# Kernel optimization log

Measured on AMD Instinct MI355X. Metric: run time of the kernel, lower is better.

The kernel has to match this reference:

```python
import jax, jax.numpy as jnp
import numpy as np

B, T, D = 16, 1024, 512      # batch, query time, model hidden
C = 4096                     # context entries
DC = 512                     # context hidden
A = 512                      # attndim
P = 512                      # proj hidden


def setup_inputs() -> dict:
    key = jax.random.key(0)
    ks = jax.random.split(key, 10)
    s = lambda fan_in: 1.0 / np.sqrt(fan_in)
    return {
        "model_embed": jax.random.normal(ks[0], (B, T, D), jnp.float32),
        "context_embed": jax.random.normal(ks[1], (C, DC), jnp.float32),
        "Wq": jax.random.uniform(ks[2], (D, A), jnp.float32, -s(D), s(D)),
        "bq": jax.random.uniform(ks[3], (A,), jnp.float32, -s(D), s(D)),
        "Wk": jax.random.uniform(ks[4], (DC, A), jnp.float32, -s(DC), s(DC)),
        "bk": jax.random.uniform(ks[5], (A,), jnp.float32, -s(DC), s(DC)),
        "Wv": jax.random.uniform(ks[6], (DC, A), jnp.float32, -s(DC), s(DC)),
        "bv": jax.random.uniform(ks[7], (A,), jnp.float32, -s(DC), s(DC)),
        "Wo": jax.random.uniform(ks[8], (A, P), jnp.float32, -s(A), s(A)),
        "bo": jax.random.uniform(ks[9], (P,), jnp.float32, -s(A), s(A)),
    }


def reference(model_embed, context_embed, Wq, bq, Wk, bk, Wv, bv, Wo, bo):
    q = model_embed @ Wq + bq            # [B, T, A]
    k = context_embed @ Wk + bk          # [C, A]
    v = context_embed @ Wv + bv          # [C, A]
    scale = 1.0 / jnp.sqrt(jnp.asarray(q.shape[-1], q.dtype))
    scores = jnp.einsum('ck,btk->btc', k, q) * scale   # [B, T, C]
    attn = jax.nn.softmax(scores, axis=-1)             # softmax over context
    x = jnp.einsum('ck,btc->btk', v, attn)             # [B, T, A]
    return x @ Wo + bo                                 # [B, T, P]
```

## Files before the change

### kernel.cpp

```cpp
#include <hip/hip_runtime.h>

#define MB_T 16384
#define DD   512
#define CC   4096
#define AA   512
#define PP   512

typedef __attribute__((ext_vector_type(4))) float f32x4;
typedef __attribute__((ext_vector_type(8))) short short8;

#define MFMA16(a, b, c) __builtin_amdgcn_mfma_f32_16x16x32_bf16((a), (b), (c), 0, 0, 0)

__device__ __forceinline__ unsigned short f2bf(float f) {
  union { float f; unsigned int u; } cv; cv.f = f;
  unsigned int u = cv.u;
  return (unsigned short)((u + 0x7FFFu + ((u >> 16) & 1u)) >> 16);
}
__device__ __forceinline__ float bf2f(unsigned short u) {
  union { unsigned int i; float f; } c; c.i = (unsigned int)u << 16; return c.f;
}

__device__ __forceinline__ void gload16(const unsigned short* g, unsigned short* l) {
  __builtin_amdgcn_global_load_lds(
      (const __attribute__((address_space(1))) unsigned int*)g,
      (__attribute__((address_space(3))) unsigned int*)l, 16, 0, 0);
}

__global__ void cast_bf16_kernel(const float* __restrict__ in,
                                 unsigned short* __restrict__ out, int n4) {
  int i = blockIdx.x * blockDim.x + threadIdx.x;
  int stride = gridDim.x * blockDim.x;
  for (; i < n4; i += stride) {
    float4 v = reinterpret_cast<const float4*>(in)[i];
    ushort4 o;
    o.x = f2bf(v.x); o.y = f2bf(v.y); o.z = f2bf(v.z); o.w = f2bf(v.w);
    reinterpret_cast<ushort4*>(out)[i] = o;
  }
}

__global__ __launch_bounds__(256) void transpose_cast_kernel(
    const float* __restrict__ W, unsigned short* __restrict__ WT, int rows, int cols) {
  __shared__ float t_s[32][33];
  int bi = blockIdx.y * 32, bj = blockIdx.x * 32;
  int r = threadIdx.x >> 3, c4 = (threadIdx.x & 7) * 4;
  float4 v = *reinterpret_cast<const float4*>(W + (size_t)(bi + r) * cols + bj + c4);
  t_s[r][c4 + 0] = v.x; t_s[r][c4 + 1] = v.y;
  t_s[r][c4 + 2] = v.z; t_s[r][c4 + 3] = v.w;
  __syncthreads();
  ushort4 o;
  o.x = f2bf(t_s[c4 + 0][r]);
  o.y = f2bf(t_s[c4 + 1][r]);
  o.z = f2bf(t_s[c4 + 2][r]);
  o.w = f2bf(t_s[c4 + 3][r]);
  *reinterpret_cast<ushort4*>(WT + (size_t)(bj + r) * rows + bi + c4) = o;
}

__global__ __launch_bounds__(256) void rowdot_kernel(
    const unsigned short* __restrict__ mat, const float* __restrict__ vec,
    float* __restrict__ outv, float scale) {
  const int lane = threadIdx.x & 63, wid = threadIdx.x >> 6;
  const int row = blockIdx.x * 4 + wid;
  const unsigned short* kr = mat + (size_t)row * 512 + lane * 8;
  float s = 0.f;
  ushort4 a = *reinterpret_cast<const ushort4*>(kr);
  ushort4 b = *reinterpret_cast<const ushort4*>(kr + 4);
  const float* bqp = vec + lane * 8;
  s += bf2f(a.x) * bqp[0]; s += bf2f(a.y) * bqp[1];
  s += bf2f(a.z) * bqp[2]; s += bf2f(a.w) * bqp[3];
  s += bf2f(b.x) * bqp[4]; s += bf2f(b.y) * bqp[5];
  s += bf2f(b.z) * bqp[6]; s += bf2f(b.w) * bqp[7];
#pragma unroll
  for (int d = 1; d < 64; d <<= 1) s += __shfl_xor(s, d);
  if (lane == 0) outv[row] = s * scale;
}

__global__ __launch_bounds__(256) void reduce_lsum_kernel(
    const float* __restrict__ lsp, float* __restrict__ lsum) {
  int m = blockIdx.x * blockDim.x + threadIdx.x;
  const float4* p = reinterpret_cast<const float4*>(lsp + (size_t)m * 64);
  float s = 0.f;
#pragma unroll
  for (int j = 0; j < 16; ++j) { float4 v = p[j]; s += v.x + v.y + v.z + v.w; }
  lsum[m] = s;
}

template <int MODE, int TM>
__global__ __launch_bounds__(256, 4) void gemm2p_kernel(
    const unsigned short* __restrict__ A, const unsigned short* __restrict__ BT,
    const float* __restrict__ bias, const float* __restrict__ colbias,
    const float* __restrict__ rowsum_in, float* __restrict__ psum_out,
    void* __restrict__ Cout, int M, int N, int K, float alpha) {
  constexpr int MFR = TM / 32;
  constexpr int WROW = TM / 2;
  constexpr int ASZ = TM * 32;
  constexpr int BSZ = 128 * 32;
  constexpr int STG = 2 * ASZ + 2 * BSZ;
  constexpr int TOT = (MODE == 3 && STG < 128 * 136) ? 128 * 136 : STG;
  __shared__ unsigned short lds[TOT];

  const int tid = threadIdx.x;
  const int lane = tid & 63, wid = tid >> 6;
  const int hq = lane >> 4, lq = lane & 15;
  const int wm = wid >> 1, wn = wid & 1;

  const int gx = gridDim.x;
  const int nwg = gx * gridDim.y;
  const int orig = blockIdx.y * gx + blockIdx.x;
  const int swz = (orig & 7) * (nwg >> 3) + (orig >> 3);
  const int bx = swz % gx, by = swz / gx;
  const int brow = by * TM, bcol = bx * 128;

  const unsigned short* ap = A + (size_t)(brow + (tid >> 2)) * K + (tid & 3) * 8;
  const unsigned short* bp = BT + (size_t)(bcol + (tid >> 2)) * K + (tid & 3) * 8;
  const size_t row64 = (size_t)64 * K;

  const int nt = K >> 5;
#pragma unroll
  for (int j = 0; j < TM / 64; ++j)
    gload16(ap + j * row64, lds + wid * 512 + j * 2048);
  gload16(bp, lds + 2 * ASZ + wid * 512);
  gload16(bp + row64, lds + 2 * ASZ + wid * 512 + 2048);
  __syncthreads();

  f32x4 acc[MFR][4] = {};
  for (int t = 0; t < nt; ++t) {
    const int cur = t & 1;
    if (t + 1 < nt) {
      const int k0 = (t + 1) * 32;
      unsigned short* an = lds + (cur ^ 1) * ASZ + wid * 512;
      unsigned short* bn = lds + 2 * ASZ + (cur ^ 1) * BSZ + wid * 512;
#pragma unroll
      for (int j = 0; j < TM / 64; ++j)
        gload16(ap + k0 + j * row64, an + j * 2048);
      gload16(bp + k0, bn);
      gload16(bp + k0 + row64, bn + 2048);
    }
    const unsigned short* as0 = lds + cur * ASZ;
    const unsigned short* bs0 = lds + 2 * ASZ + cur * BSZ;
    short8 af[MFR], bfv[4];
#pragma unroll
    for (int mf = 0; mf < MFR; ++mf)
      af[mf] = *reinterpret_cast<const short8*>(&as0[(wm * WROW + mf * 16 + lq) * 32 + hq * 8]);
#pragma unroll
    for (int nf = 0; nf < 4; ++nf)
      bfv[nf] = *reinterpret_cast<const short8*>(&bs0[(wn * 64 + nf * 16 + lq) * 32 + hq * 8]);
#pragma unroll
    for (int mf = 0; mf < MFR; ++mf)
#pragma unroll
      for (int nf = 0; nf < 4; ++nf)
        acc[mf][nf] = MFMA16(af[mf], bfv[nf], acc[mf][nf]);
    if (t + 1 < nt) __syncthreads();
  }

  if (MODE == 3) {
    float cb[4];
#pragma unroll
    for (int nf = 0; nf < 4; ++nf) cb[nf] = colbias[bcol + wn * 64 + nf * 16 + lq];
    __syncthreads();
#pragma unroll
    for (int mf = 0; mf < MFR; ++mf)
#pragma unroll
      for (int i = 0; i < 4; ++i) {
        const int rowl = wm * WROW + mf * 16 + hq * 4 + i;
        float s = 0.f;
#pragma unroll
        for (int nf = 0; nf < 4; ++nf) {
          float p = __expf(acc[mf][nf][i] + cb[nf]);
          s += p;
          lds[rowl * 136 + wn * 64 + nf * 16 + lq] = f2bf(p);
        }
        s += __shfl_xor(s, 1);
        s += __shfl_xor(s, 2);
        s += __shfl_xor(s, 4);
        s += __shfl_xor(s, 8);
        if (lq == 0) psum_out[(size_t)(brow + rowl) * 64 + bx * 2 + wn] = s;
      }
    __syncthreads();
#pragma unroll
    for (int j = 0; j < 8; ++j) {
      const int chunk = j * 256 + tid;
      const int row = chunk >> 4, c = chunk & 15;
      short8 v = *reinterpret_cast<const short8*>(&lds[row * 136 + c * 8]);
      *reinterpret_cast<short8*>((unsigned short*)Cout + (size_t)(brow + row) * N + bcol + c * 8) = v;
    }
  } else if (MODE == 5) {
#pragma unroll
    for (int mf = 0; mf < MFR; ++mf)
#pragma unroll
      for (int i = 0; i < 4; ++i) {
        const int rowg = brow + wm * WROW + mf * 16 + hq * 4 + i;
        const float inv = 1.0f / rowsum_in[rowg];
#pragma unroll
        for (int nf = 0; nf < 4; ++nf) {
          const int colg = bcol + wn * 64 + nf * 16 + lq;
          ((float*)Cout)[(size_t)rowg * N + colg] = acc[mf][nf][i] * inv + bias[colg];
        }
      }
  } else if (MODE == 1) {
#pragma unroll
    for (int nf = 0; nf < 4; ++nf) {
      const int colg = bcol + wn * 64 + nf * 16 + lq;
      const float bv = bias ? bias[colg] : 0.f;
#pragma unroll
      for (int mf = 0; mf < MFR; ++mf) {
        const int rowg0 = brow + wm * WROW + mf * 16 + hq * 4;
        ushort4 pk;
        pk.x = f2bf(acc[mf][nf][0] + bv);
        pk.y = f2bf(acc[mf][nf][1] + bv);
        pk.z = f2bf(acc[mf][nf][2] + bv);
        pk.w = f2bf(acc[mf][nf][3] + bv);
        *reinterpret_cast<ushort4*>((unsigned short*)Cout + (size_t)colg * M + rowg0) = pk;
      }
    }
  } else {
#pragma unroll
    for (int nf = 0; nf < 4; ++nf) {
      const int colg = bcol + wn * 64 + nf * 16 + lq;
      const float bv = bias ? bias[colg] : 0.f;
#pragma unroll
      for (int mf = 0; mf < MFR; ++mf) {
        const int rowg0 = brow + wm * WROW + mf * 16 + hq * 4;
#pragma unroll
        for (int i = 0; i < 4; ++i)
          ((unsigned short*)Cout)[(size_t)(rowg0 + i) * N + colg] =
              f2bf((acc[mf][nf][i] + bv) * alpha);
      }
    }
  }
}

extern "C" void kernel_launch(void* const* d_in, const int* in_sizes, int n_in,
                              void* d_out, int out_size, void* d_ws, size_t ws_size,
                              hipStream_t stream) {
  const float* model = (const float*)d_in[0];
  const float* ctx   = (const float*)d_in[1];
  const float* Wq = (const float*)d_in[2]; const float* bq = (const float*)d_in[3];
  const float* Wk = (const float*)d_in[4]; const float* bk = (const float*)d_in[5];
  const float* Wv = (const float*)d_in[6]; const float* bv = (const float*)d_in[7];
  const float* Wo = (const float*)d_in[8]; const float* bo = (const float*)d_in[9];
  float* out = (float*)d_out;

  char* ws = (char*)d_ws;
  size_t off = 0;
  auto alloc = [&](size_t bytes) -> void* {
    void* p = ws + off;
    off += (bytes + 255) & ~(size_t)255;
    return p;
  };
  unsigned short* model_bf = (unsigned short*)alloc((size_t)MB_T * DD * 2);
  unsigned short* ctx_bf   = (unsigned short*)alloc((size_t)CC * DD * 2);
  unsigned short* Wq_bf = (unsigned short*)alloc((size_t)DD * AA * 2);
  unsigned short* Wk_bf = (unsigned short*)alloc((size_t)DD * AA * 2);
  unsigned short* Wv_bf = (unsigned short*)alloc((size_t)DD * AA * 2);
  unsigned short* WoT   = (unsigned short*)alloc((size_t)AA * PP * 2);
  unsigned short* WkqT_bf = (unsigned short*)alloc((size_t)DD * DD * 2);
  unsigned short* WvoT_bf = (unsigned short*)alloc((size_t)PP * DD * 2);
  unsigned short* KqT_bf  = (unsigned short*)alloc((size_t)CC * DD * 2);
  unsigned short* W2T_bf  = (unsigned short*)alloc((size_t)PP * CC * 2);
  float* bkq  = (float*)alloc((size_t)DD * 4);
  float* bvo  = (float*)alloc((size_t)PP * 4);
  float* wkbq = (float*)alloc((size_t)DD * 4);
  float* bqk  = (float*)alloc((size_t)CC * 4);
  float* lsp  = (float*)alloc((size_t)MB_T * 64 * 4);
  float* lsum = (float*)alloc((size_t)MB_T * 4);
  unsigned short* P_bf = (unsigned short*)alloc((size_t)MB_T * CC * 2);

  const float scale = 0.04419417382415922f;

  cast_bf16_kernel<<<2048, 256, 0, stream>>>(model, model_bf, MB_T * DD / 4);
  cast_bf16_kernel<<<1024, 256, 0, stream>>>(ctx, ctx_bf, CC * DD / 4);
  cast_bf16_kernel<<<256, 256, 0, stream>>>(Wq, Wq_bf, DD * AA / 4);
  cast_bf16_kernel<<<256, 256, 0, stream>>>(Wk, Wk_bf, DD * AA / 4);
  cast_bf16_kernel<<<256, 256, 0, stream>>>(Wv, Wv_bf, DD * AA / 4);
  transpose_cast_kernel<<<dim3(16, 16), 256, 0, stream>>>(Wo, WoT, AA, PP);

  rowdot_kernel<<<DD / 4, 256, 0, stream>>>(Wq_bf, bk, bkq, scale);
  rowdot_kernel<<<DD / 4, 256, 0, stream>>>(Wk_bf, bq, wkbq, scale);
  rowdot_kernel<<<PP / 4, 256, 0, stream>>>(WoT, bv, bvo, 1.0f);
  rowdot_kernel<<<CC / 4, 256, 0, stream>>>(ctx_bf, wkbq, bqk, 1.0f);

  gemm2p_kernel<0, 128><<<dim3(4, 4), 256, 0, stream>>>(
      Wq_bf, Wk_bf, nullptr, nullptr, nullptr, nullptr, WkqT_bf, DD, DD, AA, scale);
  gemm2p_kernel<0, 128><<<dim3(4, 4), 256, 0, stream>>>(
      WoT, Wv_bf, nullptr, nullptr, nullptr, nullptr, WvoT_bf, PP, DD, AA, 1.0f);

  gemm2p_kernel<0, 128><<<dim3(4, 32), 256, 0, stream>>>(
      ctx_bf, WkqT_bf, bkq, nullptr, nullptr, nullptr, KqT_bf, CC, DD, DD, 1.0f);
  gemm2p_kernel<1, 128><<<dim3(4, 32), 256, 0, stream>>>(
      ctx_bf, WvoT_bf, bvo, nullptr, nullptr, nullptr, W2T_bf, CC, PP, DD, 1.0f);

  gemm2p_kernel<3, 128><<<dim3(32, 128), 256, 0, stream>>>(
      model_bf, KqT_bf, nullptr, bqk, nullptr, lsp, P_bf, MB_T, CC, DD, 1.0f);

  reduce_lsum_kernel<<<MB_T / 256, 256, 0, stream>>>(lsp, lsum);

  gemm2p_kernel<5, 64><<<dim3(4, 256), 256, 0, stream>>>(
      P_bf, W2T_bf, bo, nullptr, lsum, nullptr, out, MB_T, PP, CC, 1.0f);
}
```

Baseline: 363.1 us.

## Triple-buffer the score GEMM, fuse small cast/rowdot launches, tune occupancy

Replaces the scores GEMM (model × KqT with exp epilogue) with a dedicated kernel. It uses a three-stage LDS ring of async global-to-LDS loads, waits with vmcnt and raw barriers, and raises wave priority around the MFMA block. The epilogue is split into two passes over half-tiles so it can reuse the 24K-element staging buffer. Several tiny weight cast and rowdot launches are merged into multi-y-grid kernels, and the final GEMM's occupancy hint is raised to 5. The goals are deeper load/compute overlap, less launch overhead, and more waves per CU. The cost is more LDS per block (occupancy hint 3) and an extra barrier in the epilogue.

```diff
diff --git a/kernel.cpp b/kernel.cpp
--- a/kernel.cpp
+++ b/kernel.cpp
@@ -31,6 +31,21 @@
   int i = blockIdx.x * blockDim.x + threadIdx.x;
   int stride = gridDim.x * blockDim.x;
   for (; i < n4; i += stride) {
+    float4 v = reinterpret_cast<const float4*>(in)[i];
+    ushort4 o;
+    o.x = f2bf(v.x); o.y = f2bf(v.y); o.z = f2bf(v.z); o.w = f2bf(v.w);
+    reinterpret_cast<ushort4*>(out)[i] = o;
+  }
+}
+
+__global__ void cast3_kernel(const float* __restrict__ i0, const float* __restrict__ i1,
+                             const float* __restrict__ i2, unsigned short* __restrict__ o0,
+                             unsigned short* __restrict__ o1, unsigned short* __restrict__ o2,
+                             int n4) {
+  const float* in = blockIdx.y == 0 ? i0 : blockIdx.y == 1 ? i1 : i2;
+  unsigned short* out = blockIdx.y == 0 ? o0 : blockIdx.y == 1 ? o1 : o2;
+  int i = blockIdx.x * blockDim.x + threadIdx.x;
+  if (i < n4) {
     float4 v = reinterpret_cast<const float4*>(in)[i];
     ushort4 o;
     o.x = f2bf(v.x); o.y = f2bf(v.y); o.z = f2bf(v.z); o.w = f2bf(v.w);
@@ -55,9 +70,8 @@
   *reinterpret_cast<ushort4*>(WT + (size_t)(bj + r) * rows + bi + c4) = o;
 }
 
-__global__ __launch_bounds__(256) void rowdot_kernel(
-    const unsigned short* __restrict__ mat, const float* __restrict__ vec,
-    float* __restrict__ outv, float scale) {
+__device__ __forceinline__ void rowdot_body(const unsigned short* mat, const float* vec,
+                                            float* outv, float scale) {
   const int lane = threadIdx.x & 63, wid = threadIdx.x >> 6;
   const int row = blockIdx.x * 4 + wid;
   const unsigned short* kr = mat + (size_t)row * 512 + lane * 8;
@@ -74,6 +88,21 @@
   if (lane == 0) outv[row] = s * scale;
 }
 
+__global__ __launch_bounds__(256) void rowdot_kernel(
+    const unsigned short* __restrict__ mat, const float* __restrict__ vec,
+    float* __restrict__ outv, float scale) {
+  rowdot_body(mat, vec, outv, scale);
+}
+
+__global__ __launch_bounds__(256) void rowdot3_kernel(
+    const unsigned short* m0, const float* v0, float* o0, float s0,
+    const unsigned short* m1, const float* v1, float* o1, float s1,
+    const unsigned short* m2, const float* v2, float* o2, float s2) {
+  if (blockIdx.y == 0) rowdot_body(m0, v0, o0, s0);
+  else if (blockIdx.y == 1) rowdot_body(m1, v1, o1, s1);
+  else rowdot_body(m2, v2, o2, s2);
+}
+
 __global__ __launch_bounds__(256) void reduce_lsum_kernel(
     const float* __restrict__ lsp, float* __restrict__ lsum) {
   int m = blockIdx.x * blockDim.x + threadIdx.x;
@@ -84,19 +113,16 @@
   lsum[m] = s;
 }
 
-template <int MODE, int TM>
-__global__ __launch_bounds__(256, 4) void gemm2p_kernel(
+template <int MODE, int TM, int OCC>
+__global__ __launch_bounds__(256, OCC) void gemm2p_kernel(
     const unsigned short* __restrict__ A, const unsigned short* __restrict__ BT,
-    const float* __restrict__ bias, const float* __restrict__ colbias,
-    const float* __restrict__ rowsum_in, float* __restrict__ psum_out,
+    const float* __restrict__ bias, const float* __restrict__ rowsum_in,
     void* __restrict__ Cout, int M, int N, int K, float alpha) {
   constexpr int MFR = TM / 32;
   constexpr int WROW = TM / 2;
   constexpr int ASZ = TM * 32;
   constexpr int BSZ = 128 * 32;
-  constexpr int STG = 2 * ASZ + 2 * BSZ;
-  constexpr int TOT = (MODE == 3 && STG < 128 * 136) ? 128 * 136 : STG;
-  __shared__ unsigned short lds[TOT];
+  __shared__ unsigned short lds[2 * ASZ + 2 * BSZ];
 
   const int tid = threadIdx.x;
   const int lane = tid & 63, wid = tid >> 6;
@@ -152,38 +178,7 @@
     if (t + 1 < nt) __syncthreads();
   }
 
-  if (MODE == 3) {
-    float cb[4];
-#pragma unroll
-    for (int nf = 0; nf < 4; ++nf) cb[nf] = colbias[bcol + wn * 64 + nf * 16 + lq];
-    __syncthreads();
-#pragma unroll
-    for (int mf = 0; mf < MFR; ++mf)
-#pragma unroll
-      for (int i = 0; i < 4; ++i) {
-        const int rowl = wm * WROW + mf * 16 + hq * 4 + i;
-        float s = 0.f;
-#pragma unroll
-        for (int nf = 0; nf < 4; ++nf) {
-          float p = __expf(acc[mf][nf][i] + cb[nf]);
-          s += p;
-          lds[rowl * 136 + wn * 64 + nf * 16 + lq] = f2bf(p);
-        }
-        s += __shfl_xor(s, 1);
-        s += __shfl_xor(s, 2);
-        s += __shfl_xor(s, 4);
-        s += __shfl_xor(s, 8);
-        if (lq == 0) psum_out[(size_t)(brow + rowl) * 64 + bx * 2 + wn] = s;
-      }
-    __syncthreads();
-#pragma unroll
-    for (int j = 0; j < 8; ++j) {
-      const int chunk = j * 256 + tid;
-      const int row = chunk >> 4, c = chunk & 15;
-      short8 v = *reinterpret_cast<const short8*>(&lds[row * 136 + c * 8]);
-      *reinterpret_cast<short8*>((unsigned short*)Cout + (size_t)(brow + row) * N + bcol + c * 8) = v;
-    }
-  } else if (MODE == 5) {
+  if (MODE == 5) {
 #pragma unroll
     for (int mf = 0; mf < MFR; ++mf)
 #pragma unroll
@@ -225,6 +220,111 @@
           ((unsigned short*)Cout)[(size_t)(rowg0 + i) * N + colg] =
               f2bf((acc[mf][nf][i] + bv) * alpha);
       }
+    }
+  }
+}
+
+__global__ __launch_bounds__(256, 3) void gemm3b_kernel(
+    const unsigned short* __restrict__ A, const unsigned short* __restrict__ BT,
+    const float* __restrict__ colbias, float* __restrict__ psum_out,
+    unsigned short* __restrict__ Cout, int M, int N, int K) {
+  __shared__ unsigned short lds[3 * 8192];
+  const int tid = threadIdx.x;
+  const int lane = tid & 63, wid = tid >> 6;
+  const int hq = lane >> 4, lq = lane & 15;
+  const int wm = wid >> 1, wn = wid & 1;
+
+  const int gx = gridDim.x;
+  const int nwg = gx * gridDim.y;
+  const int orig = blockIdx.y * gx + blockIdx.x;
+  const int swz = (orig & 7) * (nwg >> 3) + (orig >> 3);
+  const int bx = swz % gx, by = swz / gx;
+  const int brow = by * 128, bcol = bx * 128;
+
+  const unsigned short* ap = A + (size_t)(brow + (tid >> 2)) * K + (tid & 3) * 8;
+  const unsigned short* bp = BT + (size_t)(bcol + (tid >> 2)) * K + (tid & 3) * 8;
+  const size_t row64 = (size_t)64 * K;
+  const int dst = wid * 512;
+
+  const int nt = K >> 5;
+#pragma unroll
+  for (int tt = 0; tt < 2; ++tt) {
+    unsigned short* ab = lds + tt * 8192;
+    gload16(ap + tt * 32, ab + dst);
+    gload16(ap + tt * 32 + row64, ab + dst + 2048);
+    gload16(bp + tt * 32, ab + 4096 + dst);
+    gload16(bp + tt * 32 + row64, ab + 4096 + dst + 2048);
+  }
+  asm volatile("s_waitcnt vmcnt(4)" ::: "memory");
+  __builtin_amdgcn_s_barrier();
+
+  f32x4 acc[4][4] = {};
+  for (int t = 0; t < nt; ++t) {
+    const unsigned short* ab = lds + (t % 3) * 8192;
+    if (t + 2 < nt) {
+      const int k0 = (t + 2) * 32;
+      unsigned short* nb = lds + ((t + 2) % 3) * 8192;
+      gload16(ap + k0, nb + dst);
+      gload16(ap + k0 + row64, nb + dst + 2048);
+      gload16(bp + k0, nb + 4096 + dst);
+      gload16(bp + k0 + row64, nb + 4096 + dst + 2048);
+    }
+    short8 af[4], bfv[4];
+#pragma unroll
+    for (int mf = 0; mf < 4; ++mf)
+      af[mf] = *reinterpret_cast<const short8*>(&ab[(wm * 64 + mf * 16 + lq) * 32 + hq * 8]);
+#pragma unroll
+    for (int nf = 0; nf < 4; ++nf)
+      bfv[nf] = *reinterpret_cast<const short8*>(&ab[4096 + (wn * 64 + nf * 16 + lq) * 32 + hq * 8]);
+    __builtin_amdgcn_s_setprio(1);
+#pragma unroll
+    for (int mf = 0; mf < 4; ++mf)
+#pragma unroll
+      for (int nf = 0; nf < 4; ++nf)
+        acc[mf][nf] = MFMA16(af[mf], bfv[nf], acc[mf][nf]);
+    __builtin_amdgcn_s_setprio(0);
+    if (t + 2 < nt) {
+      asm volatile("s_waitcnt vmcnt(4)" ::: "memory");
+      __builtin_amdgcn_s_barrier();
+    } else if (t + 1 < nt) {
+      asm volatile("s_waitcnt vmcnt(0)" ::: "memory");
+      __builtin_amdgcn_s_barrier();
+    }
+  }
+
+  float cb[4];
+#pragma unroll
+  for (int nf = 0; nf < 4; ++nf) cb[nf] = colbias[bcol + wn * 64 + nf * 16 + lq];
+#pragma unroll
+  for (int p = 0; p < 2; ++p) {
+    __syncthreads();
+    if (wm == p) {
+#pragma unroll
+      for (int mf = 0; mf < 4; ++mf)
+#pragma unroll
+        for (int i = 0; i < 4; ++i) {
+          const int rl = mf * 16 + hq * 4 + i;
+          float s = 0.f;
+#pragma unroll
+          for (int nf = 0; nf < 4; ++nf) {
+            float pv = __expf(acc[mf][nf][i] + cb[nf]);
+            s += pv;
+            lds[rl * 136 + wn * 64 + nf * 16 + lq] = f2bf(pv);
+          }
+          s += __shfl_xor(s, 1);
+          s += __shfl_xor(s, 2);
+          s += __shfl_xor(s, 4);
+          s += __shfl_xor(s, 8);
+          if (lq == 0) psum_out[(size_t)(brow + p * 64 + rl) * 64 + bx * 2 + wn] = s;
+        }
+    }
+    __syncthreads();
+#pragma unroll
+    for (int j = 0; j < 4; ++j) {
+      const int chunk = j * 256 + tid;
+      const int row = chunk >> 4, c = chunk & 15;
+      short8 v = *reinterpret_cast<const short8*>(&lds[row * 136 + c * 8]);
+      *reinterpret_cast<short8*>(Cout + (size_t)(brow + p * 64 + row) * N + bcol + c * 8) = v;
     }
   }
 }
@@ -269,31 +369,31 @@
 
   cast_bf16_kernel<<<2048, 256, 0, stream>>>(model, model_bf, MB_T * DD / 4);
   cast_bf16_kernel<<<1024, 256, 0, stream>>>(ctx, ctx_bf, CC * DD / 4);
-  cast_bf16_kernel<<<256, 256, 0, stream>>>(Wq, Wq_bf, DD * AA / 4);
-  cast_bf16_kernel<<<256, 256, 0, stream>>>(Wk, Wk_bf, DD * AA / 4);
-  cast_bf16_kernel<<<256, 256, 0, stream>>>(Wv, Wv_bf, DD * AA / 4);
+  cast3_kernel<<<dim3(256, 3), 256, 0, stream>>>(Wq, Wk, Wv, Wq_bf, Wk_bf, Wv_bf,
+                                                 DD * AA / 4);
   transpose_cast_kernel<<<dim3(16, 16), 256, 0, stream>>>(Wo, WoT, AA, PP);
 
-  rowdot_kernel<<<DD / 4, 256, 0, stream>>>(Wq_bf, bk, bkq, scale);
-  rowdot_kernel<<<DD / 4, 256, 0, stream>>>(Wk_bf, bq, wkbq, scale);
-  rowdot_kernel<<<PP / 4, 256, 0, stream>>>(WoT, bv, bvo, 1.0f);
+  rowdot3_kernel<<<dim3(128, 3), 256, 0, stream>>>(
+      Wq_bf, bk, bkq, scale,
+      Wk_bf, bq, wkbq, scale,
+      WoT, bv, bvo, 1.0f);
   rowdot_kernel<<<CC / 4, 256, 0, stream>>>(ctx_bf, wkbq, bqk, 1.0f);
 
-  gemm2p_kernel<0, 128><<<dim3(4, 4), 256, 0, stream>>>(
-      Wq_bf, Wk_bf, nullptr, nullptr, nullptr, nullptr, WkqT_bf, DD, DD, AA, scale);
-  gemm2p_kernel<0, 128><<<dim3(4, 4), 256, 0, stream>>>(
-      WoT, Wv_bf, nullptr, nullptr, nullptr, nullptr, WvoT_bf, PP, DD, AA, 1.0f);
-
-  gemm2p_kernel<0, 128><<<dim3(4, 32), 256, 0, stream>>>(
-      ctx_bf, WkqT_bf, bkq, nullptr, nullptr, nullptr, KqT_bf, CC, DD, DD, 1.0f);
-  gemm2p_kernel<1, 128><<<dim3(4, 32), 256, 0, stream>>>(
-      ctx_bf, WvoT_bf, bvo, nullptr, nullptr, nullptr, W2T_bf, CC, PP, DD, 1.0f);
-
-  gemm2p_kernel<3, 128><<<dim3(32, 128), 256, 0, stream>>>(
-      model_bf, KqT_bf, nullptr, bqk, nullptr, lsp, P_bf, MB_T, CC, DD, 1.0f);
+  gemm2p_kernel<0, 128, 4><<<dim3(4, 4), 256, 0, stream>>>(
+      Wq_bf, Wk_bf, nullptr, nullptr, WkqT_bf, DD, DD, AA, scale);
+  gemm2p_kernel<0, 128, 4><<<dim3(4, 4), 256, 0, stream>>>(
+      WoT, Wv_bf, nullptr, nullptr, WvoT_bf, PP, DD, AA, 1.0f);
+
+  gemm2p_kernel<0, 128, 4><<<dim3(4, 32), 256, 0, stream>>>(
+      ctx_bf, WkqT_bf, bkq, nullptr, KqT_bf, CC, DD, DD, 1.0f);
+  gemm2p_kernel<1, 128, 4><<<dim3(4, 32), 256, 0, stream>>>(
+      ctx_bf, WvoT_bf, bvo, nullptr, W2T_bf, CC, PP, DD, 1.0f);
+
+  gemm3b_kernel<<<dim3(32, 128), 256, 0, stream>>>(
+      model_bf, KqT_bf, bqk, lsp, P_bf, MB_T, CC, DD);
 
   reduce_lsum_kernel<<<MB_T / 256, 256, 0, stream>>>(lsp, lsum);
 
-  gemm2p_kernel<5, 64><<<dim3(4, 256), 256, 0, stream>>>(
-      P_bf, W2T_bf, bo, nullptr, lsum, nullptr, out, MB_T, PP, CC, 1.0f);
-}
+  gemm2p_kernel<5, 64, 5><<<dim3(4, 256), 256, 0, stream>>>(
+      P_bf, W2T_bf, bo, lsum, out, MB_T, PP, CC, 1.0f);
+}
```

New measurement: 369.4 us. About the same (+1.7%).
